# Optimization experiments

Hardware: AMD Instinct MI355X
Metric: run time of the kernel (lower is better)

Reference implementation:

```python
import math
import jax, jax.numpy as jnp
import numpy as np

T, B, E, H = 2048, 1, 2048, 32
HD = E // H          # head_dim = 64
HALF = HD // 2       # rotary half = 32
SCALE_LENGTH = 1024


def duplicate_interleave(m):
    # [S, HALF] -> [S, HD], each column duplicated adjacently
    return jnp.repeat(m, 2, axis=-1)


def rotate_every_two(x):
    # x: [BH, S, HD]
    x1 = x[:, :, ::2]
    x2 = x[:, :, 1::2]
    return jnp.stack((-x2, x1), axis=-1).reshape(x.shape)


def apply_rotary_pos_emb(x, sin, cos, scale):
    # sin/cos/scale: [S, HALF]; x: [BH, S, HD]
    sin2 = duplicate_interleave(sin * scale)
    cos2 = duplicate_interleave(cos * scale)
    return x * cos2 + rotate_every_two(x) * sin2


def setup_inputs() -> dict:
    key = jax.random.key(0)
    ks = jax.random.split(key, 8)
    std = 0.02
    query = jax.random.normal(ks[0], (T, B, E), jnp.float32)
    key_t = jax.random.normal(ks[1], (T, B, E), jnp.float32)
    value = jax.random.normal(ks[2], (T, B, E), jnp.float32)
    Wq = jax.random.normal(ks[3], (E, E), jnp.float32) * std
    Wk = jax.random.normal(ks[4], (E, E), jnp.float32) * std
    Wv = jax.random.normal(ks[5], (E, E), jnp.float32) * std
    Wo = jax.random.normal(ks[6], (E, E), jnp.float32) * std
    bq = jnp.zeros((E,), jnp.float32)
    bk = jnp.zeros((E,), jnp.float32)
    bv = jnp.zeros((E,), jnp.float32)
    bo = jnp.zeros((E,), jnp.float32)
    # XPos-style rotary tables
    pos = jnp.arange(T, dtype=jnp.float32)
    inv_freq = 1.0 / (10000.0 ** (jnp.arange(HALF, dtype=jnp.float32) / HALF))
    ang = pos[:, None] * inv_freq[None, :]          # [T, HALF]
    sin = jnp.sin(ang)
    cos = jnp.cos(ang)
    scale_base = 512.0
    dim_scale = (jnp.arange(0, HD, 2, dtype=jnp.float32) + 0.4 * HD) / (1.4 * HD)
    xscale = dim_scale[None, :] ** (pos[:, None] / scale_base)  # [T, HALF]
    # causal additive mask
    attn_mask = jnp.where(jnp.triu(jnp.ones((T, T), bool), k=1), -1e9, 0.0).astype(jnp.float32)
    return {"query": query, "key": key_t, "value": value,
            "Wq": Wq, "bq": bq, "Wk": Wk, "bk": bk, "Wv": Wv, "bv": bv,
            "Wo": Wo, "bo": bo, "sin": sin, "cos": cos, "xscale": xscale,
            "attn_mask": attn_mask, "scale_length": SCALE_LENGTH}


def reference(query, key, value, Wq, bq, Wk, bk, Wv, bv, Wo, bo,
              sin, cos, xscale, attn_mask, scale_length):
    tgt_len, bsz, embed_dim = query.shape
    scaling = HD ** -0.5

    def proj(x, W, b):
        y = x @ W.T + b                                # [T, B, E]
        return y.reshape(tgt_len, bsz * H, HD).transpose(1, 0, 2)  # [BH, T, HD]

    q = proj(query, Wq, bq)
    k = proj(key, Wk, bk)
    v = proj(value, Wv, bv)

    # self-attention XPos rotary: k scaled by 1/xscale, q by xscale (last q_len rows)
    k = apply_rotary_pos_emb(k, sin, cos, 1.0 / xscale)
    q = apply_rotary_pos_emb(q, sin[-tgt_len:], cos[-tgt_len:], xscale[-tgt_len:])

    src_len = k.shape[1]
    if src_len > scale_length:
        pos_k = jnp.arange(src_len - tgt_len, src_len, dtype=jnp.float32)
        scale_attention = jnp.maximum(1.0, jnp.log(pos_k) / math.log(scale_length))
        q = q * scale_attention[None, :, None]

    q = q * scaling
    attn_weights = jnp.einsum('btd,bsd->bts', q, k)      # [BH, T, S]
    attn_weights = attn_weights + attn_mask[None, :, :]
    attn_weights = jax.nn.softmax(attn_weights.astype(jnp.float32), axis=-1
                                  ).astype(q.dtype)
    attn = jnp.einsum('bts,bsd->btd', attn_weights, v)   # [BH, T, HD]
    attn = attn.transpose(1, 0, 2).reshape(tgt_len, bsz, embed_dim)
    attn = attn @ Wo.T + bo
    return attn
```

## Files before the change

### kernel.cpp

```cpp
#include <hip/hip_runtime.h>
#include <hip/hip_bf16.h>
#include <math.h>

#define T_LEN 2048
#define EMB   2048
#define NH    32
#define HD    64
#define HALF  32

typedef __attribute__((ext_vector_type(8))) short short8v;
typedef __attribute__((ext_vector_type(4))) float floatx4;

__device__ inline void gload_lds16(const void* g, void* l) {
    __builtin_amdgcn_global_load_lds(
        (const __attribute__((address_space(1))) unsigned int*)g,
        (__attribute__((address_space(3))) unsigned int*)l,
        16, 0, 0);
}

__device__ inline ushort f2bf(float x) {
    union { float f; unsigned u; } c; c.f = x;
    const unsigned r = c.u + 0x7FFFu + ((c.u >> 16) & 1u);
    return (ushort)(r >> 16);
}

#define BARRIER() do { asm volatile("" ::: "memory"); \
    __builtin_amdgcn_s_barrier(); asm volatile("" ::: "memory"); } while (0)
#define VMW4() asm volatile("s_waitcnt vmcnt(4)" ::: "memory")

__global__ __launch_bounds__(256) void conv_all(
    const float* __restrict__ s0, const float* __restrict__ s1,
    const float* __restrict__ s2, const float* __restrict__ s3,
    const float* __restrict__ s4, const float* __restrict__ s5,
    const float* __restrict__ s6, ushort* __restrict__ dst)
{
    const int idx = blockIdx.x * 256 + threadIdx.x;
    const int t = idx >> 19;
    const int r = (idx & 524287) * 8;
    const float* in = t == 0 ? s0 : t == 1 ? s1 : t == 2 ? s2 : t == 3 ? s3
                    : t == 4 ? s4 : t == 5 ? s5 : s6;
    const float4 v0 = *reinterpret_cast<const float4*>(&in[r]);
    const float4 v1 = *reinterpret_cast<const float4*>(&in[r + 4]);
    ushort o[8];
    o[0] = f2bf(v0.x); o[1] = f2bf(v0.y); o[2] = f2bf(v0.z); o[3] = f2bf(v0.w);
    o[4] = f2bf(v1.x); o[5] = f2bf(v1.y); o[6] = f2bf(v1.z); o[7] = f2bf(v1.w);
    *reinterpret_cast<uint4*>(&dst[(size_t)t * 4194304 + r]) =
        *reinterpret_cast<const uint4*>(o);
}

#define QBM 256
#define QBN 256
#define QBK 64

#define STAGE_A(tau, h) do {                                                   \
    const int _tc = ((tau) & 31) * 64;                                         \
    _Pragma("unroll") for (int _i = 0; _i < 2; ++_i) {                         \
        gload_lds16(&Ap[(size_t)(bm + (h) * 128 + wid * 16 + _i * 8 + rl) * 2048 + _tc + csw], \
                    &lds[((tau) & 1) * 16384 + (h) * 8192 + (wid * 16 + _i * 8) * 64]); \
    } } while (0)

#define STAGE_B(tau, h) do {                                                   \
    const int _tc = ((tau) & 31) * 64;                                         \
    _Pragma("unroll") for (int _i = 0; _i < 2; ++_i) {                         \
        gload_lds16(&Bp[(size_t)(bn + (h) * 128 + wid * 16 + _i * 8 + rl) * 2048 + _tc + csw], \
                    &lds[32768 + ((tau) & 1) * 16384 + (h) * 8192 + (wid * 16 + _i * 8) * 64]); \
    } } while (0)

#define PH(slot, mp, VMWSTMT, ...) do {                                        \
    if ((mp) == 0) {                                                           \
        _Pragma("unroll") for (int n = 0; n < 4; ++n) {                        \
            bf[n][0] = ldB(slot, n, 0);                                        \
            bf[n][1] = ldB(slot, n, 1);                                        \
        }                                                                      \
    }                                                                          \
    af[0][0] = ldA(slot, (mp) * 2, 0);     af[0][1] = ldA(slot, (mp) * 2, 1);  \
    af[1][0] = ldA(slot, (mp) * 2 + 1, 0); af[1][1] = ldA(slot, (mp) * 2 + 1, 1); \
    __VA_ARGS__;                                                               \
    BARRIER();                                                                 \
    __builtin_amdgcn_s_setprio(1);                                             \
    _Pragma("unroll") for (int mm = 0; mm < 2; ++mm)                           \
    _Pragma("unroll") for (int n = 0; n < 4; ++n)                              \
    _Pragma("unroll") for (int kk = 0; kk < 2; ++kk)                           \
        acc[(mp) * 2 + mm][n] = __builtin_amdgcn_mfma_f32_16x16x32_bf16(       \
            af[mm][kk], bf[n][kk], acc[(mp) * 2 + mm][n], 0, 0, 0);            \
    __builtin_amdgcn_s_setprio(0);                                             \
    VMWSTMT;                                                                   \
    BARRIER();                                                                 \
} while (0)

__global__ __launch_bounds__(512, 2) void gemm_qkv8(
    const ushort* __restrict__ Astack,
    const ushort* __restrict__ Wstack,
    const float* __restrict__ bq, const float* __restrict__ bk,
    const float* __restrict__ bv,
    ushort* __restrict__ outQ, ushort* __restrict__ outK,
    ushort* __restrict__ outVt,
    const float* __restrict__ sinp, const float* __restrict__ cosp,
    const float* __restrict__ xscale)
{
    __shared__ ushort lds[65536];
    const int tid  = threadIdx.x;
    const int lane = tid & 63;
    const int wid  = tid >> 6;

    const int b   = blockIdx.x + blockIdx.y * 24;
    const int xcd = b & 7;
    const int idx = b >> 3;
    const int bx  = xcd * 3 + (idx >> 3);
    const int by  = idx & 7;
    const int which = bx >> 3;
    const int bn  = (bx & 7) * QBN;
    const int bm  = by * QBM;
    const ushort* Ap = Astack + (size_t)which * 4194304;
    const ushort* Bp = Wstack + (size_t)which * 4194304;

    const int rl  = lane >> 3;
    const int csw = (((lane & 7) ^ ((lane >> 3) & 7)) * 8);
    const int lm  = lane & 15;
    const int lg  = lane >> 4;
    const char* ldsb = reinterpret_cast<const char*>(lds);

    auto ldA = [&](int slot, int m, int kk) -> short8v {
        const int row = m * 16 + lm;
        const int off = (slot * 16384 + (wid >> 2) * 8192) * 2 + row * 128
                      + (((kk * 4 + lg) ^ (row & 7)) * 16);
        return *reinterpret_cast<const short8v*>(ldsb + off);
    };
    auto ldB = [&](int slot, int n, int kk) -> short8v {
        const int row = (wid & 1) * 64 + n * 16 + lm;
        const int off = (32768 + slot * 16384 + ((wid & 3) >> 1) * 8192) * 2
                      + row * 128 + (((kk * 4 + lg) ^ (row & 7)) * 16);
        return *reinterpret_cast<const short8v*>(ldsb + off);
    };

    floatx4 acc[8][4] = {};
    short8v bf[4][2];
    short8v af[2][2];

    STAGE_A(0, 0); STAGE_A(0, 1);
    STAGE_B(0, 0); STAGE_B(0, 1);
    STAGE_B(1, 0); STAGE_B(1, 1);
    VMW4();
    BARRIER();

    for (int i = 0; i < 16; ++i) {
        const int t = 2 * i;
        PH(0, 0, (void)0, STAGE_A(t + 1, 0));
        PH(0, 1, (void)0, STAGE_A(t + 1, 1));
        PH(0, 2, (void)0, STAGE_B(t + 2, 0));
        PH(0, 3, VMW4(),  STAGE_B(t + 2, 1));
        PH(1, 0, (void)0, STAGE_A(t + 2, 0));
        PH(1, 1, (void)0, STAGE_A(t + 2, 1));
        PH(1, 2, (void)0, STAGE_B(t + 3, 0));
        PH(1, 3, VMW4(),  STAGE_B(t + 3, 1));
    }
    asm volatile("s_waitcnt vmcnt(0)" ::: "memory");

    const float* bias = which == 0 ? bq : which == 1 ? bk : bv;
    #pragma unroll
    for (int m = 0; m < 8; ++m) {
        #pragma unroll
        for (int n = 0; n < 4; ++n) {
            const int col = bn + (wid & 3) * 64 + n * 16 + lm;
            const float bz = bias[col];
            const int row0 = bm + (wid >> 2) * 128 + m * 16 + lg * 4;
            if (which == 2) {
                ushort o4[4];
                #pragma unroll
                for (int j = 0; j < 4; ++j)
                    o4[j] = f2bf(acc[m][n][j] + bz);
                *reinterpret_cast<uint2*>(&outVt[(size_t)col * T_LEN + row0]) =
                    *reinterpret_cast<const uint2*>(o4);
            } else {
                ushort* O = which == 0 ? outQ : outK;
                const int p = (col & 63) >> 1;
                const bool even = (col & 1) == 0;
                #pragma unroll
                for (int j = 0; j < 4; ++j) {
                    const int row = row0 + j;
                    const float v = acc[m][n][j] + bz;
                    const float pv = __shfl_xor(v, 1);
                    const float s  = sinp[row * HALF + p];
                    const float c  = cosp[row * HALF + p];
                    const float xs = xscale[row * HALF + p];
                    float scale;
                    if (which == 0) {
                        float sa = 1.f;
                        if (row >= 2) {
                            const float lv = __logf((float)row) * 0.14426950408889634f;
                            sa = lv > 1.f ? lv : 1.f;
                        }
                        scale = xs * sa * 0.125f;
                    } else {
                        scale = 1.0f / xs;
                    }
                    const float C_ = c * scale, S_ = s * scale;
                    const float outv = even ? v * C_ - pv * S_ : v * C_ + pv * S_;
                    O[(size_t)row * EMB + col] = f2bf(outv);
                }
            }
        }
    }
}

#define GBM 128
#define GBN 128
#define GBK 64

__global__ __launch_bounds__(256) void gemm_out(
    const ushort* __restrict__ A,
    const ushort* __restrict__ B,
    const float* __restrict__ bias,
    float* __restrict__ C)
{
    __shared__ ushort As[GBM * GBK];
    __shared__ ushort Bs[GBN * GBK];
    const int tid  = threadIdx.x;
    const int lane = tid & 63;
    const int wid  = tid >> 6;
    const int bm = blockIdx.y * GBM;
    const int bn = blockIdx.x * GBN;
    const int wr = (wid >> 1) * 64;
    const int wc = (wid & 1) * 64;

    floatx4 acc[4][4] = {};

    const int lrow  = lane >> 3;
    const int lcolb = (lane & 7) * 8;

    for (int k0 = 0; k0 < EMB; k0 += GBK) {
        #pragma unroll
        for (int c = 0; c < 4; ++c) {
            const int chunk = wid * 4 + c;
            const int row = chunk * 8 + lrow;
            gload_lds16(&A[(size_t)(bm + row) * EMB + k0 + lcolb], &As[chunk * 512]);
            gload_lds16(&B[(size_t)(bn + row) * EMB + k0 + lcolb], &Bs[chunk * 512]);
        }
        __syncthreads();
        #pragma unroll
        for (int kk = 0; kk < 2; ++kk) {
            short8v a[4], b[4];
            #pragma unroll
            for (int m = 0; m < 4; ++m)
                a[m] = *reinterpret_cast<const short8v*>(
                    &As[(wr + m * 16 + (lane & 15)) * GBK + kk * 32 + (lane >> 4) * 8]);
            #pragma unroll
            for (int n = 0; n < 4; ++n)
                b[n] = *reinterpret_cast<const short8v*>(
                    &Bs[(wc + n * 16 + (lane & 15)) * GBK + kk * 32 + (lane >> 4) * 8]);
            #pragma unroll
            for (int m = 0; m < 4; ++m)
                #pragma unroll
                for (int n = 0; n < 4; ++n)
                    acc[m][n] = __builtin_amdgcn_mfma_f32_16x16x32_bf16(
                        a[m], b[n], acc[m][n], 0, 0, 0);
        }
        __syncthreads();
    }

    const int cr = (lane >> 4) * 4;
    const int cc = lane & 15;
    #pragma unroll
    for (int m = 0; m < 4; ++m) {
        #pragma unroll
        for (int n = 0; n < 4; ++n) {
            const int col = bn + wc + n * 16 + cc;
            const float bz = bias[col];
            #pragma unroll
            for (int j = 0; j < 4; ++j) {
                const int row = bm + wr + m * 16 + cr + j;
                C[(size_t)row * EMB + col] = acc[m][n][j] + bz;
            }
        }
    }
}

__global__ __launch_bounds__(256) void flash_attn_mfma(
    const ushort* __restrict__ Qb,
    const ushort* __restrict__ Kb,
    const ushort* __restrict__ Vt,
    ushort* __restrict__ Ob)
{
    __shared__ ushort Ks[2][64 * 64];
    __shared__ ushort Vs[2][64 * 64];
    __shared__ ushort Ps[4][16 * 64];

    const int h   = blockIdx.x;
    const int qb  = (T_LEN / 64 - 1) - blockIdx.y;
    const int tid = threadIdx.x;
    const int lane = tid & 63;
    const int wid  = tid >> 6;
    const int qrow_w = qb * 64 + wid * 16;
    const int lm = lane & 15;
    const int lg = lane >> 4;

    short8v qf[2];
    {
        const ushort* qp = &Qb[(size_t)(qrow_w + lm) * EMB + h * HD + lg * 8];
        qf[0] = *reinterpret_cast<const short8v*>(qp);
        qf[1] = *reinterpret_cast<const short8v*>(qp + 32);
    }

    floatx4 oacc[4] = {};
    float m = -1e30f, l = 0.f;

    const int srow = lane >> 3;
    const int schk = lane & 7;

    {
        #pragma unroll
        for (int i = 0; i < 2; ++i) {
            const int slot = wid * 2 + i;
            const int row  = slot * 8 + srow;
            const int cswz = (schk ^ (row & 7)) * 8;
            gload_lds16(&Kb[(size_t)row * EMB + h * HD + cswz], &Ks[0][slot * 512]);
            gload_lds16(&Vt[(size_t)(h * HD + row) * T_LEN + cswz], &Vs[0][slot * 512]);
        }
    }
    __syncthreads();

    for (int kb = 0; kb <= qb; ++kb) {
        const int cur = kb & 1;
        if (kb < qb) {
            const int nkb = kb + 1;
            #pragma unroll
            for (int i = 0; i < 2; ++i) {
                const int slot = wid * 2 + i;
                const int row  = slot * 8 + srow;
                const int cswz = (schk ^ (row & 7)) * 8;
                gload_lds16(&Kb[(size_t)(nkb * 64 + row) * EMB + h * HD + cswz],
                            &Ks[cur ^ 1][slot * 512]);
                gload_lds16(&Vt[(size_t)(h * HD + row) * T_LEN + nkb * 64 + cswz],
                            &Vs[cur ^ 1][slot * 512]);
            }
        }

        float sv[16];
        #pragma unroll
        for (int t = 0; t < 4; ++t) {
            floatx4 sacc = {};
            const int srow_l = t * 16 + lm;
            const char* krow = reinterpret_cast<const char*>(Ks[cur]) + srow_l * 128;
            const int swz = (srow_l & 7) << 4;
            #pragma unroll
            for (int kk = 0; kk < 2; ++kk) {
                const int cb = (kk * 64 + lg * 16) ^ swz;
                short8v kf = *reinterpret_cast<const short8v*>(krow + cb);
                sacc = __builtin_amdgcn_mfma_f32_16x16x32_bf16(kf, qf[kk], sacc, 0, 0, 0);
            }
            sv[t * 4 + 0] = sacc[0]; sv[t * 4 + 1] = sacc[1];
            sv[t * 4 + 2] = sacc[2]; sv[t * 4 + 3] = sacc[3];
        }

        const int qg = qrow_w + lm;
        if (kb == qb) {
            #pragma unroll
            for (int t = 0; t < 4; ++t)
                #pragma unroll
                for (int r = 0; r < 4; ++r) {
                    const int sg = kb * 64 + t * 16 + lg * 4 + r;
                    if (sg > qg) sv[t * 4 + r] = -1e30f;
                }
        }

        float mx = sv[0];
        #pragma unroll
        for (int i = 1; i < 16; ++i) mx = fmaxf(mx, sv[i]);
        mx = fmaxf(mx, __shfl_xor(mx, 16));
        mx = fmaxf(mx, __shfl_xor(mx, 32));
        float corr = 1.f;
        if (!__all(mx - m <= 8.f)) {
            const float mnew = fmaxf(m, mx);
            corr = __expf(m - mnew);
            m = mnew;
            float corr4[4];
            #pragma unroll
            for (int r = 0; r < 4; ++r)
                corr4[r] = __shfl(corr, lg * 4 + r);
            #pragma unroll
            for (int td = 0; td < 4; ++td)
                #pragma unroll
                for (int r = 0; r < 4; ++r)
                    oacc[td][r] *= corr4[r];
        }
        float ps = 0.f;
        unsigned pw[8];
        #pragma unroll
        for (int i = 0; i < 8; ++i) {
            const float p0 = __expf(sv[2 * i + 0] - m);
            const float p1 = __expf(sv[2 * i + 1] - m);
            ps += p0 + p1;
            const __hip_bfloat162 h2 = __float22bfloat162_rn(make_float2(p0, p1));
            pw[i] = *reinterpret_cast<const unsigned*>(&h2);
        }
        ps += __shfl_xor(ps, 16);
        ps += __shfl_xor(ps, 32);
        l = l * corr + ps;

        {
            char* pbase = reinterpret_cast<char*>(&Ps[wid][0]) + lm * 128;
            const int swz = (lm & 7) << 4;
            #pragma unroll
            for (int t = 0; t < 4; ++t) {
                uint2 w;
                w.x = pw[2 * t + 0];
                w.y = pw[2 * t + 1];
                const int cb = (t * 32 + lg * 8) ^ swz;
                *reinterpret_cast<uint2*>(pbase + cb) = w;
            }
        }

        const char* pwave = reinterpret_cast<const char*>(&Ps[wid][0]);
        #pragma unroll
        for (int kk = 0; kk < 2; ++kk) {
            const int acb = (kk * 64 + lg * 16) ^ ((lm & 7) << 4);
            short8v pa = *reinterpret_cast<const short8v*>(pwave + lm * 128 + acb);
            #pragma unroll
            for (int td = 0; td < 4; ++td) {
                const int d = td * 16 + lm;
                const int bcb = (kk * 64 + lg * 16) ^ ((d & 7) << 4);
                short8v vb = *reinterpret_cast<const short8v*>(
                    reinterpret_cast<const char*>(Vs[cur]) + d * 128 + bcb);
                oacc[td] = __builtin_amdgcn_mfma_f32_16x16x32_bf16(pa, vb, oacc[td], 0, 0, 0);
            }
        }

        __syncthreads();
    }

    float invl[4];
    #pragma unroll
    for (int r = 0; r < 4; ++r)
        invl[r] = 1.f / __shfl(l, lg * 4 + r);
    #pragma unroll
    for (int td = 0; td < 4; ++td) {
        #pragma unroll
        for (int r = 0; r < 4; ++r) {
            const int trow = qrow_w + lg * 4 + r;
            const int col  = h * HD + td * 16 + lm;
            Ob[(size_t)trow * EMB + col] = f2bf(oacc[td][r] * invl[r]);
        }
    }
}

extern "C" void kernel_launch(void* const* d_in, const int* in_sizes, int n_in,
                              void* d_out, int out_size, void* d_ws, size_t ws_size,
                              hipStream_t stream) {
    const float* query = (const float*)d_in[0];
    const float* key   = (const float*)d_in[1];
    const float* value = (const float*)d_in[2];
    const float* Wq = (const float*)d_in[3];
    const float* bq = (const float*)d_in[4];
    const float* Wk = (const float*)d_in[5];
    const float* bk = (const float*)d_in[6];
    const float* Wv = (const float*)d_in[7];
    const float* bv = (const float*)d_in[8];
    const float* Wo = (const float*)d_in[9];
    const float* bo = (const float*)d_in[10];
    const float* sinp   = (const float*)d_in[11];
    const float* cosp   = (const float*)d_in[12];
    const float* xscale = (const float*)d_in[13];
    float* out = (float*)d_out;

    const size_t MB = 1024 * 1024;
    char* ws = (char*)d_ws;
    ushort* bWqkv = (ushort*)(ws + 0 * MB);
    ushort* bWo   = (ushort*)(ws + 24 * MB);
    ushort* bAqkv = (ushort*)(ws + 32 * MB);
    ushort* bQ  = (ushort*)(ws + 56 * MB);
    ushort* bK  = (ushort*)(ws + 64 * MB);
    ushort* bVt = (ushort*)(ws + 72 * MB);
    ushort* bAo = (ushort*)(ws + 80 * MB);

    conv_all<<<7 * 524288 / 256, 256, 0, stream>>>(
        Wq, Wk, Wv, Wo, query, key, value, bWqkv);

    dim3 gQKV(24, 8);
    gemm_qkv8<<<gQKV, 512, 0, stream>>>(bAqkv, bWqkv, bq, bk, bv,
                                        bQ, bK, bVt, sinp, cosp, xscale);

    dim3 gFlash(NH, T_LEN / 64);
    flash_attn_mfma<<<gFlash, 256, 0, stream>>>(bQ, bK, bVt, bAo);

    dim3 gGemm(EMB / GBN, T_LEN / GBM);
    gemm_out<<<gGemm, 256, 0, stream>>>(bAo, bWo, bo, out);
}
```

Baseline: 198.4 us.

## Triple-buffer A tiles in QKV GEMM, precompute rotary tables, use exp2 softmax

Result: slower. 435.1 us (+119.3%).

```diff
diff --git a/kernel.cpp b/kernel.cpp
--- a/kernel.cpp
+++ b/kernel.cpp
@@ -26,7 +26,8 @@
 
 #define BARRIER() do { asm volatile("" ::: "memory"); \
     __builtin_amdgcn_s_barrier(); asm volatile("" ::: "memory"); } while (0)
-#define VMW4() asm volatile("s_waitcnt vmcnt(4)" ::: "memory")
+#define VMW8() asm volatile("s_waitcnt vmcnt(8)" ::: "memory")
+#define VMW0() asm volatile("s_waitcnt vmcnt(0)" ::: "memory")
 
 __global__ __launch_bounds__(256) void conv_all(
     const float* __restrict__ s0, const float* __restrict__ s1,
@@ -48,33 +49,51 @@
         *reinterpret_cast<const uint4*>(o);
 }
 
+__global__ __launch_bounds__(256) void rot_tables(
+    const float* __restrict__ sinp, const float* __restrict__ cosp,
+    const float* __restrict__ xscale,
+    float2* __restrict__ qt, float2* __restrict__ kt)
+{
+    const int idx = blockIdx.x * 256 + threadIdx.x;
+    const int t = idx >> 5;
+    const float s = sinp[idx], c = cosp[idx], xs = xscale[idx];
+    float sa = 1.f;
+    if (t >= 2) {
+        const float lv = __logf((float)t) * 0.14426950408889634f;
+        sa = lv > 1.f ? lv : 1.f;
+    }
+    const float qs = xs * sa * 0.125f * 1.4426950408889634f;
+    qt[idx] = make_float2(c * qs, s * qs);
+    const float ks = 1.f / xs;
+    kt[idx] = make_float2(c * ks, s * ks);
+}
+
 #define QBM 256
 #define QBN 256
-#define QBK 64
-
-#define STAGE_A(tau, h) do {                                                   \
-    const int _tc = ((tau) & 31) * 64;                                         \
+
+#define STAGE_A3(tau, h, slot) do {                                            \
+    const int _tc = (tau) * 64;                                                \
     _Pragma("unroll") for (int _i = 0; _i < 2; ++_i) {                         \
         gload_lds16(&Ap[(size_t)(bm + (h) * 128 + wid * 16 + _i * 8 + rl) * 2048 + _tc + csw], \
-                    &lds[((tau) & 1) * 16384 + (h) * 8192 + (wid * 16 + _i * 8) * 64]); \
+                    &lds[(slot) * 16384 + (h) * 8192 + (wid * 16 + _i * 8) * 64]); \
     } } while (0)
 
-#define STAGE_B(tau, h) do {                                                   \
-    const int _tc = ((tau) & 31) * 64;                                         \
+#define STAGE_B2(tau, h) do {                                                  \
+    const int _tc = (tau) * 64;                                                \
     _Pragma("unroll") for (int _i = 0; _i < 2; ++_i) {                         \
         gload_lds16(&Bp[(size_t)(bn + (h) * 128 + wid * 16 + _i * 8 + rl) * 2048 + _tc + csw], \
-                    &lds[32768 + ((tau) & 1) * 16384 + (h) * 8192 + (wid * 16 + _i * 8) * 64]); \
+                    &lds[49152 + ((tau) & 1) * 16384 + (h) * 8192 + (wid * 16 + _i * 8) * 64]); \
     } } while (0)
 
-#define PH(slot, mp, VMWSTMT, ...) do {                                        \
+#define PH(sa_, sb_, mp, VMWSTMT, ...) do {                                    \
     if ((mp) == 0) {                                                           \
         _Pragma("unroll") for (int n = 0; n < 4; ++n) {                        \
-            bf[n][0] = ldB(slot, n, 0);                                        \
-            bf[n][1] = ldB(slot, n, 1);                                        \
+            bf[n][0] = ldB(sb_, n, 0);                                         \
+            bf[n][1] = ldB(sb_, n, 1);                                         \
         }                                                                      \
     }                                                                          \
-    af[0][0] = ldA(slot, (mp) * 2, 0);     af[0][1] = ldA(slot, (mp) * 2, 1);  \
-    af[1][0] = ldA(slot, (mp) * 2 + 1, 0); af[1][1] = ldA(slot, (mp) * 2 + 1, 1); \
+    af[0][0] = ldA(sa_, (mp) * 2, 0);     af[0][1] = ldA(sa_, (mp) * 2, 1);    \
+    af[1][0] = ldA(sa_, (mp) * 2 + 1, 0); af[1][1] = ldA(sa_, (mp) * 2 + 1, 1);\
     __VA_ARGS__;                                                               \
     BARRIER();                                                                 \
     __builtin_amdgcn_s_setprio(1);                                             \
@@ -95,10 +114,9 @@
     const float* __restrict__ bv,
     ushort* __restrict__ outQ, ushort* __restrict__ outK,
     ushort* __restrict__ outVt,
-    const float* __restrict__ sinp, const float* __restrict__ cosp,
-    const float* __restrict__ xscale)
+    const float2* __restrict__ qtab, const float2* __restrict__ ktab)
 {
-    __shared__ ushort lds[65536];
+    __shared__ ushort lds[81920];
     const int tid  = threadIdx.x;
     const int lane = tid & 63;
     const int wid  = tid >> 6;
@@ -128,7 +146,7 @@
     };
     auto ldB = [&](int slot, int n, int kk) -> short8v {
         const int row = (wid & 1) * 64 + n * 16 + lm;
-        const int off = (32768 + slot * 16384 + ((wid & 3) >> 1) * 8192) * 2
+        const int off = (49152 + slot * 16384 + ((wid & 3) >> 1) * 8192) * 2
                       + row * 128 + (((kk * 4 + lg) ^ (row & 7)) * 16);
         return *reinterpret_cast<const short8v*>(ldsb + off);
     };
@@ -137,26 +155,33 @@
     short8v bf[4][2];
     short8v af[2][2];
 
-    STAGE_A(0, 0); STAGE_A(0, 1);
-    STAGE_B(0, 0); STAGE_B(0, 1);
-    STAGE_B(1, 0); STAGE_B(1, 1);
-    VMW4();
+    STAGE_A3(0, 0, 0); STAGE_A3(0, 1, 0);
+    STAGE_B2(0, 0);    STAGE_B2(0, 1);
+    STAGE_A3(1, 0, 1); STAGE_A3(1, 1, 1);
+    STAGE_B2(1, 0);    STAGE_B2(1, 1);
+    VMW8();
     BARRIER();
 
-    for (int i = 0; i < 16; ++i) {
-        const int t = 2 * i;
-        PH(0, 0, (void)0, STAGE_A(t + 1, 0));
-        PH(0, 1, (void)0, STAGE_A(t + 1, 1));
-        PH(0, 2, (void)0, STAGE_B(t + 2, 0));
-        PH(0, 3, VMW4(),  STAGE_B(t + 2, 1));
-        PH(1, 0, (void)0, STAGE_A(t + 2, 0));
-        PH(1, 1, (void)0, STAGE_A(t + 2, 1));
-        PH(1, 2, (void)0, STAGE_B(t + 3, 0));
-        PH(1, 3, VMW4(),  STAGE_B(t + 3, 1));
-    }
-    asm volatile("s_waitcnt vmcnt(0)" ::: "memory");
+    int sa0 = 0, sa1 = 1, sa2 = 2;
+    for (int t = 0; t < 32; ++t) {
+        const int sb = t & 1;
+        if (t < 30) {
+            PH(sa0, sb, 0, (void)0, STAGE_A3(t + 2, 0, sa2));
+            PH(sa0, sb, 1, (void)0, STAGE_A3(t + 2, 1, sa2));
+            PH(sa0, sb, 2, (void)0, STAGE_B2(t + 2, 0));
+            if (t == 29) { PH(sa0, sb, 3, VMW0(), STAGE_B2(t + 2, 1)); }
+            else         { PH(sa0, sb, 3, VMW8(), STAGE_B2(t + 2, 1)); }
+        } else {
+            PH(sa0, sb, 0, (void)0, (void)0);
+            PH(sa0, sb, 1, (void)0, (void)0);
+            PH(sa0, sb, 2, (void)0, (void)0);
+            PH(sa0, sb, 3, (void)0, (void)0);
+        }
+        const int tmp = sa0; sa0 = sa1; sa1 = sa2; sa2 = tmp;
+    }
 
     const float* bias = which == 0 ? bq : which == 1 ? bk : bv;
+    const float2* tbl = which == 0 ? qtab : ktab;
     #pragma unroll
     for (int m = 0; m < 8; ++m) {
         #pragma unroll
@@ -180,22 +205,9 @@
                     const int row = row0 + j;
                     const float v = acc[m][n][j] + bz;
                     const float pv = __shfl_xor(v, 1);
-                    const float s  = sinp[row * HALF + p];
-                    const float c  = cosp[row * HALF + p];
-                    const float xs = xscale[row * HALF + p];
-                    float scale;
-                    if (which == 0) {
-                        float sa = 1.f;
-                        if (row >= 2) {
-                            const float lv = __logf((float)row) * 0.14426950408889634f;
-                            sa = lv > 1.f ? lv : 1.f;
-                        }
-                        scale = xs * sa * 0.125f;
-                    } else {
-                        scale = 1.0f / xs;
-                    }
-                    const float C_ = c * scale, S_ = s * scale;
-                    const float outv = even ? v * C_ - pv * S_ : v * C_ + pv * S_;
+                    const float2 cs = tbl[row * HALF + p];
+                    const float outv = even ? v * cs.x - pv * cs.y
+                                            : v * cs.x + pv * cs.y;
                     O[(size_t)row * EMB + col] = f2bf(outv);
                 }
             }
@@ -369,9 +381,9 @@
         mx = fmaxf(mx, __shfl_xor(mx, 16));
         mx = fmaxf(mx, __shfl_xor(mx, 32));
         float corr = 1.f;
-        if (!__all(mx - m <= 8.f)) {
+        if (!__all(mx - m <= 11.544f)) {
             const float mnew = fmaxf(m, mx);
-            corr = __expf(m - mnew);
+            corr = exp2f(m - mnew);
             m = mnew;
             float corr4[4];
             #pragma unroll
@@ -387,8 +399,8 @@
         unsigned pw[8];
         #pragma unroll
         for (int i = 0; i < 8; ++i) {
-            const float p0 = __expf(sv[2 * i + 0] - m);
-            const float p1 = __expf(sv[2 * i + 1] - m);
+            const float p0 = exp2f(sv[2 * i + 0] - m);
+            const float p1 = exp2f(sv[2 * i + 1] - m);
             ps += p0 + p1;
             const __hip_bfloat162 h2 = __float22bfloat162_rn(make_float2(p0, p1));
             pw[i] = *reinterpret_cast<const unsigned*>(&h2);
@@ -471,13 +483,17 @@
     ushort* bK  = (ushort*)(ws + 64 * MB);
     ushort* bVt = (ushort*)(ws + 72 * MB);
     ushort* bAo = (ushort*)(ws + 80 * MB);
+    float2* qtab = (float2*)(ws + 88 * MB);
+    float2* ktab = (float2*)(ws + 88 * MB + 512 * 1024);
 
     conv_all<<<7 * 524288 / 256, 256, 0, stream>>>(
         Wq, Wk, Wv, Wo, query, key, value, bWqkv);
+    rot_tables<<<T_LEN * HALF / 256, 256, 0, stream>>>(
+        sinp, cosp, xscale, qtab, ktab);
 
     dim3 gQKV(24, 8);
     gemm_qkv8<<<gQKV, 512, 0, stream>>>(bAqkv, bWqkv, bq, bk, bv,
-                                        bQ, bK, bVt, sinp, cosp, xscale);
+                                        bQ, bK, bVt, qtab, ktab);
 
     dim3 gFlash(NH, T_LEN / 64);
     flash_attn_mfma<<<gFlash, 256, 0, stream>>>(bQ, bK, bVt, bAo);
```
